# Kernel tuning notes

Measured on AMD Instinct MI355X. Metric: run time of the kernel, lower is better.

The kernel has to match this reference:

```python
import jax, jax.numpy as jnp
import numpy as np

H, W = 32, 32
C = 512
HEADS = 8
HEAD_DIM = C // HEADS
B = 8
GROUPS = 32
EPS = 1e-6
N = H * W


def _rel_indices():
    # (N, N) lookup indices into the (2H-1)*(2W-1) relative-position table
    y = np.arange(H)
    x = np.arange(W)
    y1, x1, y2, x2 = np.meshgrid(y, x, y, x, indexing='ij')
    idx = (y1 - y2 + H - 1) * (2 * W - 1) + (x1 - x2 + W - 1)
    return jnp.asarray(idx.reshape(N, N), dtype=jnp.int32)

REL_IDX = _rel_indices()


def setup_inputs() -> dict:
    key = jax.random.key(0)
    ks = jax.random.split(key, 8)
    s = 0.02
    return {
        'x': jax.random.normal(ks[0], (B, C, H, W), jnp.float32),
        '_1': jnp.zeros((1,), jnp.int32),
        '_2': jnp.zeros((1,), jnp.int32),
        'gamma': jnp.ones((C,), jnp.float32),
        'beta': jnp.zeros((C,), jnp.float32),
        'wq': jax.random.normal(ks[1], (C, C), jnp.float32) * s,
        'bq': jnp.zeros((C,), jnp.float32),
        'wk': jax.random.normal(ks[2], (C, C), jnp.float32) * s,
        'bk': jnp.zeros((C,), jnp.float32),
        'wv': jax.random.normal(ks[3], (C, C), jnp.float32) * s,
        'bv': jnp.zeros((C,), jnp.float32),
        'wproj': jax.random.normal(ks[4], (C, C), jnp.float32) * s,
        'bproj': jnp.zeros((C,), jnp.float32),
        'pos_enc': jax.random.normal(ks[5], (HEADS, (2 * H - 1) * (2 * W - 1)), jnp.float32) * s,
    }


def _group_norm(x, gamma, beta):
    b, c, h, w = x.shape
    xg = x.reshape(b, GROUPS, c // GROUPS, h, w)
    mean = xg.mean(axis=(2, 3, 4), keepdims=True)
    var = xg.var(axis=(2, 3, 4), keepdims=True)
    xg = (xg - mean) * jax.lax.rsqrt(var + EPS)
    x = xg.reshape(b, c, h, w)
    return x * gamma[None, :, None, None] + beta[None, :, None, None]


def reference(x, _1, _2, gamma, beta, wq, bq, wk, bk, wv, bv, wproj, bproj, pos_enc):
    x0 = x
    xn = _group_norm(x, gamma, beta)
    xt = xn.reshape(B, C, N)  # (B, C, N)

    def proj(w, bias):
        # 1x1 conv == channel matmul: (B, C_out, N)
        y = jnp.einsum('oc,bcn->bon', w, xt) + bias[None, :, None]
        # split heads: channel index = head*HEAD_DIM + d -> (B, heads, N, d)
        return y.reshape(B, HEADS, HEAD_DIM, N).transpose(0, 1, 3, 2)

    q = proj(wq, bq)
    k = proj(wk, bk)
    v = proj(wv, bv)

    scale = 1.0 / jnp.sqrt(jnp.float32(HEAD_DIM))
    attn = jnp.einsum('bhqd,bhkd->bhqk', q, k) * scale  # (B, heads, N, N)
    rel_bias = pos_enc[:, REL_IDX]  # (heads, N, N)
    attn = attn + rel_bias[None]
    attn = jax.nn.softmax(attn, axis=-1)

    out = jnp.einsum('bhqk,bhkd->bhqd', attn, v)  # (B, heads, N, d)
    out = out.transpose(0, 1, 3, 2).reshape(B, C, H, W)
    out = jnp.einsum('oc,bchw->bohw', wproj, out) + bproj[None, :, None, None]
    return out + x0
```

## Files before the change

### kernel.cpp

```cpp
#include <hip/hip_runtime.h>
#include <hip/hip_bf16.h>
#include <math.h>

typedef __bf16 bf16_t;
typedef __bf16 bf16x8 __attribute__((ext_vector_type(8)));
typedef __bf16 bf16x4 __attribute__((ext_vector_type(4)));
typedef float  f32x4  __attribute__((ext_vector_type(4)));

#define MFMA16(a, b, c) __builtin_amdgcn_mfma_f32_16x16x32_bf16((a), (b), (c), 0, 0, 0)
#define GLDS16(g, s) __builtin_amdgcn_global_load_lds( \
    (const __attribute__((address_space(1))) void*)(g), \
    (__attribute__((address_space(3))) void*)(s), 16, 0, 0)

#define LOG2E 1.4426950408889634f

__global__ __launch_bounds__(256) void cast_weights(
    const float* __restrict__ wq, const float* __restrict__ wk,
    const float* __restrict__ wv, const float* __restrict__ wp,
    bf16_t* __restrict__ Wqkv, bf16_t* __restrict__ Wp)
{
    const int i = (blockIdx.x * 256 + threadIdx.x) * 4;
#pragma unroll
    for (int j = 0; j < 4; ++j) {
        Wqkv[i + j]          = (bf16_t)wq[i + j];
        Wqkv[262144 + i + j] = (bf16_t)wk[i + j];
        Wqkv[524288 + i + j] = (bf16_t)wv[i + j];
        Wp[i + j]            = (bf16_t)wp[i + j];
    }
}

__global__ __launch_bounds__(256) void bias_kernel(
    const float* __restrict__ pos, bf16_t* __restrict__ Bias2)
{
    const int h   = blockIdx.x >> 6;
    const int qt  = blockIdx.x & 63;
    const int qy  = qt >> 1;
    const int qxb = (qt & 1) * 16;
    const int t = threadIdx.x;
    __shared__ bf16_t ps[32][64];

    for (int i = t; i < 32 * 63; i += 256) {
        const int r = i / 63, dx = i - r * 63;
        ps[r][dx] = (bf16_t)(pos[h * 3969 + (qy + r) * 63 + dx] * LOG2E);
    }
    __syncthreads();

    bf16_t* outb = Bias2 + (((size_t)h * 64 + qt) * 64) * 256;
#pragma unroll
    for (int it = 0; it < 16; ++it) {
        const int idx = t + it * 256;
        const int kt = idx >> 6, l = idx & 63;
        const int qx  = qxb + (l & 15);
        const int nk0 = kt * 16 + (l >> 4) * 4;
        const int ky = nk0 >> 5;
        const int kx0 = nk0 & 31;
        const int r = 31 - ky;
        const int dx0 = qx - kx0 + 31;
        bf16x4 o;
#pragma unroll
        for (int j = 0; j < 4; ++j) o[j] = ps[r][dx0 - j];
        *(bf16x4*)(outb + (size_t)idx * 4) = o;
    }
}

__global__ __launch_bounds__(512) void gn_kernel(
    const float* __restrict__ x, const float* __restrict__ gamma,
    const float* __restrict__ beta, bf16_t* __restrict__ xnT)
{
    const int blk = blockIdx.x;
    const int b = blk >> 5, g = blk & 31;
    const int t = threadIdx.x;
    const int hi = t >> 8, tl = t & 255;
    __shared__ float red[16];
    const float* base = x + ((size_t)b * 512 + g * 16) * 1024;

    f32x4 v[8];
    float s = 0.f, s2 = 0.f;
#pragma unroll
    for (int it = 0; it < 8; ++it) {
        v[it] = *(const f32x4*)(base + (size_t)hi * 8192 + it * 1024 + tl * 4);
#pragma unroll
        for (int j = 0; j < 4; ++j) { s += v[it][j]; s2 += v[it][j] * v[it][j]; }
    }
#pragma unroll
    for (int m = 1; m < 64; m <<= 1) { s += __shfl_xor(s, m); s2 += __shfl_xor(s2, m); }
    const int w = t >> 6;
    if ((t & 63) == 0) { red[w] = s; red[8 + w] = s2; }
    __syncthreads();
    s = 0.f; s2 = 0.f;
#pragma unroll
    for (int i = 0; i < 8; ++i) { s += red[i]; s2 += red[8 + i]; }
    const float mean = s * (1.f / 16384.f);
    const float var  = fmaxf(s2 * (1.f / 16384.f) - mean * mean, 0.f);
    const float rstd = rsqrtf(var + 1e-6f);

    float ga[8], be[8];
#pragma unroll
    for (int it = 0; it < 8; ++it) {
        const int gc = g * 16 + hi * 8 + it;
        ga[it] = gamma[gc] * rstd;
        be[it] = beta[gc] - mean * ga[it];
    }
#pragma unroll
    for (int j = 0; j < 4; ++j) {
        bf16x8 o;
#pragma unroll
        for (int it = 0; it < 8; ++it)
            o[it] = (bf16_t)(v[it][j] * ga[it] + be[it]);
        *(bf16x8*)(xnT + ((size_t)b * 1024 + tl * 4 + j) * 512 + g * 16 + hi * 8) = o;
    }
}

__global__ __launch_bounds__(256) void gemm_bt(
    const bf16_t* __restrict__ A, const bf16_t* __restrict__ Bt, int mode,
    int mtiles,
    const float* __restrict__ bias0, const float* __restrict__ bias1,
    const float* __restrict__ bias2,
    const float* __restrict__ x0, float* __restrict__ outF,
    bf16_t* __restrict__ Qb, bf16_t* __restrict__ Kb, bf16_t* __restrict__ Vb)
{
    const int K  = 512;
    const int g  = blockIdx.x;
    const int xcd = g & 7;
    const int i_  = g >> 3;
    const int m_idx = i_ % mtiles;
    const int n_idx = xcd * 8 + i_ / mtiles;
    const int m0 = m_idx * 128;
    const int n0 = n_idx * 128;
    const int t = threadIdx.x;
    const int l = t & 63, w = t >> 6;
    const int wr = w >> 1, wc = w & 1;
    const int lrow = l & 15, lgrp = l >> 4;

    __shared__ __align__(16) char smem_raw[49152];
    bf16_t* Ct = (bf16_t*)smem_raw;

    f32x4 acc[4][4];
#pragma unroll
    for (int i = 0; i < 4; ++i)
#pragma unroll
        for (int j = 0; j < 4; ++j) acc[i][j] = (f32x4){0.f, 0.f, 0.f, 0.f};

    const bf16_t* gA0 = A  + (size_t)(m0 + w * 16 + (l >> 2)) * K + (l & 3) * 8;
    const bf16_t* gA1 = gA0 + (size_t)64 * K;
    const bf16_t* gB0 = Bt + (size_t)(n0 + w * 16 + (l >> 2)) * K + (l & 3) * 8;
    const bf16_t* gB1 = gB0 + (size_t)64 * K;

#define STAGE(s, k0) do {                                                   \
    bf16_t* As_ = (bf16_t*)(smem_raw + (s) * 16384);                        \
    bf16_t* Bs_ = (bf16_t*)(smem_raw + (s) * 16384 + 8192);                 \
    GLDS16(gA0 + (k0), As_ + w * 512);                                      \
    GLDS16(gA1 + (k0), As_ + 2048 + w * 512);                               \
    GLDS16(gB0 + (k0), Bs_ + w * 512);                                      \
    GLDS16(gB1 + (k0), Bs_ + 2048 + w * 512); } while (0)

    STAGE(0, 0);
    STAGE(1, 32);

#pragma unroll
    for (int tk = 0; tk < 16; ++tk) {
        if (tk < 15) asm volatile("s_waitcnt vmcnt(4)" ::: "memory");
        else         asm volatile("s_waitcnt vmcnt(0)" ::: "memory");
        __builtin_amdgcn_s_barrier();
        __builtin_amdgcn_sched_barrier(0);
        if (tk + 2 < 16) STAGE((tk + 2) % 3, (tk + 2) * 32);
        const bf16_t* Asb = (const bf16_t*)(smem_raw + (tk % 3) * 16384);
        const bf16_t* Bsb = Asb + 4096;
        bf16x8 af[4], bfr[4];
#pragma unroll
        for (int ms = 0; ms < 4; ++ms)
            af[ms] = *(const bf16x8*)&Asb[(wr * 64 + ms * 16 + lrow) * 32 + lgrp * 8];
#pragma unroll
        for (int ns = 0; ns < 4; ++ns)
            bfr[ns] = *(const bf16x8*)&Bsb[(wc * 64 + ns * 16 + lrow) * 32 + lgrp * 8];
        __builtin_amdgcn_s_setprio(1);
#pragma unroll
        for (int ms = 0; ms < 4; ++ms)
#pragma unroll
            for (int ns = 0; ns < 4; ++ns)
                acc[ms][ns] = MFMA16(af[ms], bfr[ns], acc[ms][ns]);
        __builtin_amdgcn_s_setprio(0);
    }
#undef STAGE

    if (mode == 0) {
        const int which = m0 >> 9;
        const int mq = (m0 >> 7) & 3;
        const float* bias = (which == 0) ? bias0 : (which == 1) ? bias1 : bias2;
        const float scl = (which == 0) ? 0.125f * LOG2E : 1.0f;
        const int b   = n_idx >> 3;
        const int nn0 = (n_idx & 7) * 128;

        __syncthreads();
        if (which < 2) {
            bf16_t* Qk = (which == 0) ? Qb : Kb;
#pragma unroll
            for (int ms = 0; ms < 4; ++ms) {
                const int ml = wr * 64 + ms * 16 + lgrp * 4;
#pragma unroll
                for (int ns = 0; ns < 4; ++ns) {
                    const int nl = wc * 64 + ns * 16 + lrow;
                    bf16x4 pk;
#pragma unroll
                    for (int j = 0; j < 4; ++j)
                        pk[j] = (bf16_t)((acc[ms][ns][j] + bias[mq * 128 + ml + j]) * scl);
                    *(bf16x4*)&Ct[nl * 136 + ml] = pk;
                }
            }
            __syncthreads();
#pragma unroll
            for (int it = 0; it < 8; ++it) {
                const int idx = it * 256 + t;
                const int token = idx >> 4, oc = idx & 15;
                const bf16x8 vv8 = *(const bf16x8*)&Ct[token * 136 + oc * 8];
                const int head = mq * 2 + (oc >> 3);
                const int d = (oc & 7) * 8;
                *(bf16x8*)(Qk + (((size_t)b * 8 + head) * 1024 + nn0 + token) * 64 + d) = vv8;
            }
        } else {
#pragma unroll
            for (int ms = 0; ms < 4; ++ms) {
                const int ml = wr * 64 + ms * 16 + lgrp * 4;
#pragma unroll
                for (int ns = 0; ns < 4; ++ns) {
                    const int nl = wc * 64 + ns * 16 + lrow;
#pragma unroll
                    for (int j = 0; j < 4; ++j)
                        Ct[(ml + j) * 136 + nl] =
                            (bf16_t)(acc[ms][ns][j] + bias[mq * 128 + ml + j]);
                }
            }
            __syncthreads();
#pragma unroll
            for (int it = 0; it < 8; ++it) {
                const int idx = it * 256 + t;
                const int o = idx >> 4, nc = idx & 15;
                const bf16x8 vv8 = *(const bf16x8*)&Ct[o * 136 + nc * 8];
                const int head = mq * 2 + (o >> 6);
                const int d = o & 63;
                *(bf16x8*)(Vb + (((size_t)b * 8 + head) * 64 + d) * 1024 + nn0 + nc * 8) = vv8;
            }
        }
    } else {
#pragma unroll
        for (int ms = 0; ms < 4; ++ms) {
#pragma unroll
            for (int ns = 0; ns < 4; ++ns) {
                const int c  = m0 + wr * 64 + ms * 16 + lgrp * 4;
                const int np = n0 + wc * 64 + ns * 16 + lrow;
                const int b = np >> 10, n = np & 1023;
#pragma unroll
                for (int j = 0; j < 4; ++j) {
                    const size_t idx = ((size_t)b * 512 + c + j) * 1024 + n;
                    outF[idx] = acc[ms][ns][j] + bias0[c + j] + x0[idx];
                }
            }
        }
    }
}

__global__ __launch_bounds__(512) void attn_kernel(
    const bf16_t* __restrict__ Qb, const bf16_t* __restrict__ Kb,
    const bf16_t* __restrict__ Vb, const bf16_t* __restrict__ Bias2,
    bf16_t* __restrict__ Xo)
{
    const int bh = blockIdx.x;
    const int h  = bh & 7;
    const int q0 = blockIdx.y * 128;
    const int t = threadIdx.x;
    const int w = t >> 6, l = t & 63;
    const int lrow = l & 15, lgrp = l >> 4;

    __shared__ __align__(16) bf16_t Ks[128][72];
    __shared__ __align__(16) bf16_t Vs[64][136];
    __shared__ __align__(16) bf16_t Ps[8][16][72];

    const int qrow = q0 + w * 16 + lrow;
    const bf16_t* qbase = Qb + ((size_t)bh * 1024 + qrow) * 64;
    const bf16x8 qf0 = *(const bf16x8*)(qbase + lgrp * 8);
    const bf16x8 qf1 = *(const bf16x8*)(qbase + 32 + lgrp * 8);

    const bf16_t* bb = Bias2 + (((size_t)h * 64 + (q0 >> 4) + w) * 64) * 256;

    bf16x8 ones;
#pragma unroll
    for (int i = 0; i < 8; ++i) ones[i] = (bf16_t)1.0f;

    f32x4 oacc[4], tsacc = (f32x4){0.f, 0.f, 0.f, 0.f};
#pragma unroll
    for (int j = 0; j < 4; ++j) oacc[j] = (f32x4){0.f, 0.f, 0.f, 0.f};

    const int sr2 = t >> 3;
    const int sc2 = (t & 7) * 8;
    const bf16_t* Kg = Kb + ((size_t)bh * 1024 + sr2) * 64 + sc2;
    const bf16_t* Vg = Vb + ((size_t)bh * 64 + sr2) * 1024 + sc2;

    bf16x8 kv0 = *(const bf16x8*)(Kg);
    bf16x8 kv1 = *(const bf16x8*)(Kg + (size_t)64 * 64);
    bf16x8 vv0 = *(const bf16x8*)(Vg);
    bf16x8 vv1 = *(const bf16x8*)(Vg + 64);
    bf16x4 bA[8], bB[8];
#pragma unroll
    for (int k = 0; k < 8; ++k)
        bA[k] = *(const bf16x4*)(bb + (size_t)(k * 64 + l) * 4);

    auto dtile = [&](int it, bf16x4 (&bcur)[8], bf16x4 (&bnxt)[8]) {
        const int nk0 = it * 128;
        __syncthreads();
        *(bf16x8*)&Ks[sr2][sc2]      = kv0;
        *(bf16x8*)&Ks[64 + sr2][sc2] = kv1;
        *(bf16x8*)&Vs[sr2][sc2]      = vv0;
        *(bf16x8*)&Vs[sr2][64 + sc2] = vv1;
        __syncthreads();
        if (it < 7) {
            const int nkn = nk0 + 128;
#pragma unroll
            for (int k = 0; k < 8; ++k)
                bnxt[k] = *(const bf16x4*)(bb + (size_t)((((nkn >> 4)) + k) * 64 + l) * 4);
            kv0 = *(const bf16x8*)(Kg + (size_t)nkn * 64);
            kv1 = *(const bf16x8*)(Kg + (size_t)(nkn + 64) * 64);
            vv0 = *(const bf16x8*)(Vg + nkn);
            vv1 = *(const bf16x8*)(Vg + nkn + 64);
        }

#pragma unroll
        for (int st = 0; st < 2; ++st) {
            f32x4 s[4];
#pragma unroll
            for (int ns = 0; ns < 4; ++ns) {
                const bf16x4 bc = bcur[st * 4 + ns];
                f32x4 z = (f32x4){(float)bc[0], (float)bc[1],
                                  (float)bc[2], (float)bc[3]};
                const bf16x8 kf0 = *(const bf16x8*)&Ks[st * 64 + ns * 16 + lrow][lgrp * 8];
                const bf16x8 kf1 = *(const bf16x8*)&Ks[st * 64 + ns * 16 + lrow][32 + lgrp * 8];
                z = MFMA16(kf0, qf0, z);
                z = MFMA16(kf1, qf1, z);
                s[ns] = z;
            }
#pragma unroll
            for (int ns = 0; ns < 4; ++ns) {
                bf16x4 pk;
                pk[0] = (bf16_t)exp2f(s[ns][0]);
                pk[1] = (bf16_t)exp2f(s[ns][1]);
                pk[2] = (bf16_t)exp2f(s[ns][2]);
                pk[3] = (bf16_t)exp2f(s[ns][3]);
                *(bf16x4*)&Ps[w][lrow][ns * 16 + lgrp * 4] = pk;
            }
            const bf16x8 pf0 = *(const bf16x8*)&Ps[w][lrow][lgrp * 8];
            const bf16x8 pf1 = *(const bf16x8*)&Ps[w][lrow][32 + lgrp * 8];
            tsacc = MFMA16(ones, pf0, tsacc);
            tsacc = MFMA16(ones, pf1, tsacc);
#pragma unroll
            for (int ds = 0; ds < 4; ++ds) {
                const bf16x8 vf0 = *(const bf16x8*)&Vs[ds * 16 + lrow][st * 64 + lgrp * 8];
                const bf16x8 vf1 = *(const bf16x8*)&Vs[ds * 16 + lrow][st * 64 + 32 + lgrp * 8];
                oacc[ds] = MFMA16(vf0, pf0, oacc[ds]);
                oacc[ds] = MFMA16(vf1, pf1, oacc[ds]);
            }
        }
    };

    for (int it2 = 0; it2 < 8; it2 += 2) {
        dtile(it2,     bA, bB);
        dtile(it2 + 1, bB, bA);
    }

    const float inv = 1.0f / tsacc[0];

    const int b = bh >> 3;
    const int q = q0 + w * 16 + lrow;
    bf16_t* xrow = Xo + ((size_t)b * 1024 + q) * 512 + h * 64;
#pragma unroll
    for (int ds = 0; ds < 4; ++ds) {
        bf16x4 o4;
#pragma unroll
        for (int j = 0; j < 4; ++j) o4[j] = (bf16_t)(oacc[ds][j] * inv);
        *(bf16x4*)(xrow + ds * 16 + lgrp * 4) = o4;
    }
}

extern "C" void kernel_launch(void* const* d_in, const int* in_sizes, int n_in,
                              void* d_out, int out_size, void* d_ws, size_t ws_size,
                              hipStream_t stream)
{
    const float* x     = (const float*)d_in[0];
    const float* gamma = (const float*)d_in[3];
    const float* beta  = (const float*)d_in[4];
    const float* wq    = (const float*)d_in[5];
    const float* bq    = (const float*)d_in[6];
    const float* wk    = (const float*)d_in[7];
    const float* bk    = (const float*)d_in[8];
    const float* wv    = (const float*)d_in[9];
    const float* bv    = (const float*)d_in[10];
    const float* wp    = (const float*)d_in[11];
    const float* bp    = (const float*)d_in[12];
    const float* pos   = (const float*)d_in[13];
    float* out = (float*)d_out;

    size_t off = 0;
    char* wsb = (char*)d_ws;
    auto alloc = [&](size_t bytes) { char* p = wsb + off; off += bytes; return p; };
    bf16_t* Wqkv  = (bf16_t*)alloc((size_t)1536 * 512 * 2);
    bf16_t* Wp    = (bf16_t*)alloc((size_t)512 * 512 * 2);
    bf16_t* xnT   = (bf16_t*)alloc((size_t)8192 * 512 * 2);
    bf16_t* Qb    = (bf16_t*)alloc((size_t)8192 * 512 * 2);
    bf16_t* Kb    = (bf16_t*)alloc((size_t)8192 * 512 * 2);
    bf16_t* Vb    = (bf16_t*)alloc((size_t)8192 * 512 * 2);
    bf16_t* Xo    = (bf16_t*)alloc((size_t)8192 * 512 * 2);
    bf16_t* Bias2 = (bf16_t*)alloc((size_t)8 * 64 * 64 * 64 * 4 * 2);

    hipLaunchKernelGGL(cast_weights, dim3(256), dim3(256), 0, stream,
                       wq, wk, wv, wp, Wqkv, Wp);
    hipLaunchKernelGGL(bias_kernel, dim3(512), dim3(256), 0, stream, pos, Bias2);
    hipLaunchKernelGGL(gn_kernel, dim3(256), dim3(512), 0, stream,
                       x, gamma, beta, xnT);
    hipLaunchKernelGGL(gemm_bt, dim3(768), dim3(256), 0, stream,
                       Wqkv, xnT, 0, 12, bq, bk, bv,
                       nullptr, nullptr, Qb, Kb, Vb);
    hipLaunchKernelGGL(attn_kernel, dim3(64, 8), dim3(512), 0, stream,
                       Qb, Kb, Vb, Bias2, Xo);
    hipLaunchKernelGGL(gemm_bt, dim3(256), dim3(256), 0, stream,
                       Wp, Xo, 1, 4, bp, nullptr, nullptr,
                       x, out, nullptr, nullptr, nullptr);
}
```

Before: 93.67 us.

## Switch attention to 32x32 MFMA with register-resident P via permlane32 swap

The attention kernel now uses 32x32x16 MFMA tiles, so each wave handles 32 query rows and each block 256 queries. The probability tile no longer round-trips through LDS; it is packed and rearranged in registers with v_permlane32_swap. The bias table is laid out again to match the 32x32 accumulator layout, and the bias kernel is rewritten to produce it. This halves K/V reloads per query and drops the LDS P traffic, at the cost of more registers per thread and only 256 attention blocks.

```diff
diff --git a/kernel.cpp b/kernel.cpp
--- a/kernel.cpp
+++ b/kernel.cpp
@@ -5,9 +5,13 @@
 typedef __bf16 bf16_t;
 typedef __bf16 bf16x8 __attribute__((ext_vector_type(8)));
 typedef __bf16 bf16x4 __attribute__((ext_vector_type(4)));
+typedef __bf16 bf16x2 __attribute__((ext_vector_type(2)));
 typedef float  f32x4  __attribute__((ext_vector_type(4)));
+typedef float  f32x16 __attribute__((ext_vector_type(16)));
+typedef unsigned u32x4 __attribute__((ext_vector_type(4)));
 
 #define MFMA16(a, b, c) __builtin_amdgcn_mfma_f32_16x16x32_bf16((a), (b), (c), 0, 0, 0)
+#define MFMA32(a, b, c) __builtin_amdgcn_mfma_f32_32x32x16_bf16((a), (b), (c), 0, 0, 0)
 #define GLDS16(g, s) __builtin_amdgcn_global_load_lds( \
     (const __attribute__((address_space(1))) void*)(g), \
     (__attribute__((address_space(3))) void*)(s), 16, 0, 0)
@@ -30,36 +34,35 @@
 }
 
 __global__ __launch_bounds__(256) void bias_kernel(
-    const float* __restrict__ pos, bf16_t* __restrict__ Bias2)
-{
-    const int h   = blockIdx.x >> 6;
-    const int qt  = blockIdx.x & 63;
-    const int qy  = qt >> 1;
-    const int qxb = (qt & 1) * 16;
+    const float* __restrict__ pos, bf16_t* __restrict__ Bias3)
+{
+    const int h  = blockIdx.x >> 5;
+    const int qt = blockIdx.x & 31;
     const int t = threadIdx.x;
+    const int l = t & 63, ko = t >> 6;
     __shared__ bf16_t ps[32][64];
 
     for (int i = t; i < 32 * 63; i += 256) {
         const int r = i / 63, dx = i - r * 63;
-        ps[r][dx] = (bf16_t)(pos[h * 3969 + (qy + r) * 63 + dx] * LOG2E);
+        ps[r][dx] = (bf16_t)(pos[h * 3969 + (qt + r) * 63 + dx] * LOG2E);
     }
     __syncthreads();
 
-    bf16_t* outb = Bias2 + (((size_t)h * 64 + qt) * 64) * 256;
-#pragma unroll
-    for (int it = 0; it < 16; ++it) {
-        const int idx = t + it * 256;
-        const int kt = idx >> 6, l = idx & 63;
-        const int qx  = qxb + (l & 15);
-        const int nk0 = kt * 16 + (l >> 4) * 4;
-        const int ky = nk0 >> 5;
-        const int kx0 = nk0 & 31;
-        const int r = 31 - ky;
-        const int dx0 = qx - kx0 + 31;
-        bf16x4 o;
-#pragma unroll
-        for (int j = 0; j < 4; ++j) o[j] = ps[r][dx0 - j];
-        *(bf16x4*)(outb + (size_t)idx * 4) = o;
+    const int qx = l & 31, hi = l >> 5;
+#pragma unroll
+    for (int kt0 = 0; kt0 < 32; kt0 += 4) {
+        const int kt = kt0 + ko;
+        const int row = 31 - kt;
+        bf16x8 o0, o1;
+#pragma unroll
+        for (int reg = 0; reg < 16; ++reg) {
+            const int kx = (reg & 3) + 8 * (reg >> 2) + 4 * hi;
+            const bf16_t v = ps[row][qx - kx + 31];
+            if (reg < 8) o0[reg] = v; else o1[reg - 8] = v;
+        }
+        bf16_t* outp = Bias3 + ((size_t)(((h * 32 + qt) * 32 + kt) * 64 + l)) * 16;
+        *(bf16x8*)outp       = o0;
+        *(bf16x8*)(outp + 8) = o1;
     }
 }
 
@@ -259,36 +262,38 @@
     }
 }
 
-__global__ __launch_bounds__(512) void attn_kernel(
+__global__ __launch_bounds__(512, 2) void attn_kernel(
     const bf16_t* __restrict__ Qb, const bf16_t* __restrict__ Kb,
-    const bf16_t* __restrict__ Vb, const bf16_t* __restrict__ Bias2,
+    const bf16_t* __restrict__ Vb, const bf16_t* __restrict__ Bias3,
     bf16_t* __restrict__ Xo)
 {
     const int bh = blockIdx.x;
     const int h  = bh & 7;
-    const int q0 = blockIdx.y * 128;
+    const int q0 = blockIdx.y * 256;
     const int t = threadIdx.x;
     const int w = t >> 6, l = t & 63;
-    const int lrow = l & 15, lgrp = l >> 4;
+    const int lq = l & 31, hi = l >> 5;
 
     __shared__ __align__(16) bf16_t Ks[128][72];
     __shared__ __align__(16) bf16_t Vs[64][136];
-    __shared__ __align__(16) bf16_t Ps[8][16][72];
-
-    const int qrow = q0 + w * 16 + lrow;
+
+    const int qrow = q0 + w * 32 + lq;
     const bf16_t* qbase = Qb + ((size_t)bh * 1024 + qrow) * 64;
-    const bf16x8 qf0 = *(const bf16x8*)(qbase + lgrp * 8);
-    const bf16x8 qf1 = *(const bf16x8*)(qbase + 32 + lgrp * 8);
-
-    const bf16_t* bb = Bias2 + (((size_t)h * 64 + (q0 >> 4) + w) * 64) * 256;
+    bf16x8 qf[4];
+#pragma unroll
+    for (int dc = 0; dc < 4; ++dc)
+        qf[dc] = *(const bf16x8*)(qbase + dc * 16 + hi * 8);
+
+    const bf16_t* bbase = Bias3 +
+        ((size_t)((h * 32 + (q0 >> 5) + w) * 32)) * 1024 + (size_t)l * 16;
 
     bf16x8 ones;
 #pragma unroll
     for (int i = 0; i < 8; ++i) ones[i] = (bf16_t)1.0f;
 
-    f32x4 oacc[4], tsacc = (f32x4){0.f, 0.f, 0.f, 0.f};
-#pragma unroll
-    for (int j = 0; j < 4; ++j) oacc[j] = (f32x4){0.f, 0.f, 0.f, 0.f};
+    f32x16 oacc[2], tsacc;
+#pragma unroll
+    for (int j = 0; j < 16; ++j) { oacc[0][j] = 0.f; oacc[1][j] = 0.f; tsacc[j] = 0.f; }
 
     const int sr2 = t >> 3;
     const int sc2 = (t & 7) * 8;
@@ -299,12 +304,14 @@
     bf16x8 kv1 = *(const bf16x8*)(Kg + (size_t)64 * 64);
     bf16x8 vv0 = *(const bf16x8*)(Vg);
     bf16x8 vv1 = *(const bf16x8*)(Vg + 64);
-    bf16x4 bA[8], bB[8];
-#pragma unroll
-    for (int k = 0; k < 8; ++k)
-        bA[k] = *(const bf16x4*)(bb + (size_t)(k * 64 + l) * 4);
-
-    auto dtile = [&](int it, bf16x4 (&bcur)[8], bf16x4 (&bnxt)[8]) {
+    bf16x8 bA[8], bB[8];
+#pragma unroll
+    for (int k = 0; k < 4; ++k) {
+        bA[2 * k]     = *(const bf16x8*)(bbase + (size_t)k * 1024);
+        bA[2 * k + 1] = *(const bf16x8*)(bbase + (size_t)k * 1024 + 8);
+    }
+
+    auto dtile = [&](int it, bf16x8 (&bcur)[8], bf16x8 (&bnxt)[8]) {
         const int nk0 = it * 128;
         __syncthreads();
         *(bf16x8*)&Ks[sr2][sc2]      = kv0;
@@ -315,8 +322,10 @@
         if (it < 7) {
             const int nkn = nk0 + 128;
 #pragma unroll
-            for (int k = 0; k < 8; ++k)
-                bnxt[k] = *(const bf16x4*)(bb + (size_t)((((nkn >> 4)) + k) * 64 + l) * 4);
+            for (int k = 0; k < 4; ++k) {
+                bnxt[2 * k]     = *(const bf16x8*)(bbase + (size_t)((it + 1) * 4 + k) * 1024);
+                bnxt[2 * k + 1] = *(const bf16x8*)(bbase + (size_t)((it + 1) * 4 + k) * 1024 + 8);
+            }
             kv0 = *(const bf16x8*)(Kg + (size_t)nkn * 64);
             kv1 = *(const bf16x8*)(Kg + (size_t)(nkn + 64) * 64);
             vv0 = *(const bf16x8*)(Vg + nkn);
@@ -324,38 +333,48 @@
         }
 
 #pragma unroll
-        for (int st = 0; st < 2; ++st) {
-            f32x4 s[4];
-#pragma unroll
-            for (int ns = 0; ns < 4; ++ns) {
-                const bf16x4 bc = bcur[st * 4 + ns];
-                f32x4 z = (f32x4){(float)bc[0], (float)bc[1],
-                                  (float)bc[2], (float)bc[3]};
-                const bf16x8 kf0 = *(const bf16x8*)&Ks[st * 64 + ns * 16 + lrow][lgrp * 8];
-                const bf16x8 kf1 = *(const bf16x8*)&Ks[st * 64 + ns * 16 + lrow][32 + lgrp * 8];
-                z = MFMA16(kf0, qf0, z);
-                z = MFMA16(kf1, qf1, z);
-                s[ns] = z;
-            }
-#pragma unroll
-            for (int ns = 0; ns < 4; ++ns) {
-                bf16x4 pk;
-                pk[0] = (bf16_t)exp2f(s[ns][0]);
-                pk[1] = (bf16_t)exp2f(s[ns][1]);
-                pk[2] = (bf16_t)exp2f(s[ns][2]);
-                pk[3] = (bf16_t)exp2f(s[ns][3]);
-                *(bf16x4*)&Ps[w][lrow][ns * 16 + lgrp * 4] = pk;
-            }
-            const bf16x8 pf0 = *(const bf16x8*)&Ps[w][lrow][lgrp * 8];
-            const bf16x8 pf1 = *(const bf16x8*)&Ps[w][lrow][32 + lgrp * 8];
-            tsacc = MFMA16(ones, pf0, tsacc);
-            tsacc = MFMA16(ones, pf1, tsacc);
-#pragma unroll
-            for (int ds = 0; ds < 4; ++ds) {
-                const bf16x8 vf0 = *(const bf16x8*)&Vs[ds * 16 + lrow][st * 64 + lgrp * 8];
-                const bf16x8 vf1 = *(const bf16x8*)&Vs[ds * 16 + lrow][st * 64 + 32 + lgrp * 8];
-                oacc[ds] = MFMA16(vf0, pf0, oacc[ds]);
-                oacc[ds] = MFMA16(vf1, pf1, oacc[ds]);
+        for (int kt = 0; kt < 4; ++kt) {
+            const int ktloc = kt * 32;
+            f32x16 sa;
+#pragma unroll
+            for (int r = 0; r < 8; ++r) {
+                sa[r]     = (float)bcur[2 * kt][r];
+                sa[8 + r] = (float)bcur[2 * kt + 1][r];
+            }
+#pragma unroll
+            for (int dc = 0; dc < 4; ++dc) {
+                const bf16x8 kf = *(const bf16x8*)&Ks[ktloc + lq][dc * 16 + hi * 8];
+                sa = MFMA32(kf, qf[dc], sa);
+            }
+            unsigned W00, W01, W10, W11, W20, W21, W30, W31;
+            {
+                float p[16];
+#pragma unroll
+                for (int r = 0; r < 16; ++r) p[r] = exp2f(sa[r]);
+                bf16x2 tw;
+#define PACKW(dst, a, b_) { tw[0] = (bf16_t)p[a]; tw[1] = (bf16_t)p[b_]; \
+                            dst = __builtin_bit_cast(unsigned, tw); }
+                PACKW(W00, 0, 1)   PACKW(W01, 2, 3)
+                PACKW(W10, 4, 5)   PACKW(W11, 6, 7)
+                PACKW(W20, 8, 9)   PACKW(W21, 10, 11)
+                PACKW(W30, 12, 13) PACKW(W31, 14, 15)
+#undef PACKW
+            }
+            asm volatile("v_permlane32_swap_b32 %0, %1" : "+v"(W00), "+v"(W10));
+            asm volatile("v_permlane32_swap_b32 %0, %1" : "+v"(W01), "+v"(W11));
+            asm volatile("v_permlane32_swap_b32 %0, %1" : "+v"(W20), "+v"(W30));
+            asm volatile("v_permlane32_swap_b32 %0, %1" : "+v"(W21), "+v"(W31));
+            const bf16x8 pf0 = __builtin_bit_cast(bf16x8, (u32x4){W00, W01, W10, W11});
+            const bf16x8 pf1 = __builtin_bit_cast(bf16x8, (u32x4){W20, W21, W30, W31});
+
+            tsacc = MFMA32(ones, pf0, tsacc);
+            tsacc = MFMA32(ones, pf1, tsacc);
+#pragma unroll
+            for (int dh = 0; dh < 2; ++dh) {
+                const bf16x8 vf0 = *(const bf16x8*)&Vs[dh * 32 + lq][ktloc + hi * 8];
+                const bf16x8 vf1 = *(const bf16x8*)&Vs[dh * 32 + lq][ktloc + 16 + hi * 8];
+                oacc[dh] = MFMA32(vf0, pf0, oacc[dh]);
+                oacc[dh] = MFMA32(vf1, pf1, oacc[dh]);
             }
         }
     };
@@ -368,15 +387,18 @@
     const float inv = 1.0f / tsacc[0];
 
     const int b = bh >> 3;
-    const int q = q0 + w * 16 + lrow;
+    const int q = q0 + w * 32 + lq;
     bf16_t* xrow = Xo + ((size_t)b * 1024 + q) * 512 + h * 64;
 #pragma unroll
-    for (int ds = 0; ds < 4; ++ds) {
-        bf16x4 o4;
-#pragma unroll
-        for (int j = 0; j < 4; ++j) o4[j] = (bf16_t)(oacc[ds][j] * inv);
-        *(bf16x4*)(xrow + ds * 16 + lgrp * 4) = o4;
-    }
+    for (int dh = 0; dh < 2; ++dh)
+#pragma unroll
+        for (int rr = 0; rr < 4; ++rr) {
+            bf16x4 o4;
+#pragma unroll
+            for (int j = 0; j < 4; ++j)
+                o4[j] = (bf16_t)(oacc[dh][4 * rr + j] * inv);
+            *(bf16x4*)(xrow + dh * 32 + 8 * rr + 4 * hi) = o4;
+        }
 }
 
 extern "C" void kernel_launch(void* const* d_in, const int* in_sizes, int n_in,
@@ -407,18 +429,18 @@
     bf16_t* Kb    = (bf16_t*)alloc((size_t)8192 * 512 * 2);
     bf16_t* Vb    = (bf16_t*)alloc((size_t)8192 * 512 * 2);
     bf16_t* Xo    = (bf16_t*)alloc((size_t)8192 * 512 * 2);
-    bf16_t* Bias2 = (bf16_t*)alloc((size_t)8 * 64 * 64 * 64 * 4 * 2);
+    bf16_t* Bias3 = (bf16_t*)alloc((size_t)8 * 32 * 32 * 64 * 16 * 2);
 
     hipLaunchKernelGGL(cast_weights, dim3(256), dim3(256), 0, stream,
                        wq, wk, wv, wp, Wqkv, Wp);
-    hipLaunchKernelGGL(bias_kernel, dim3(512), dim3(256), 0, stream, pos, Bias2);
+    hipLaunchKernelGGL(bias_kernel, dim3(256), dim3(256), 0, stream, pos, Bias3);
     hipLaunchKernelGGL(gn_kernel, dim3(256), dim3(512), 0, stream,
                        x, gamma, beta, xnT);
     hipLaunchKernelGGL(gemm_bt, dim3(768), dim3(256), 0, stream,
                        Wqkv, xnT, 0, 12, bq, bk, bv,
                        nullptr, nullptr, Qb, Kb, Vb);
-    hipLaunchKernelGGL(attn_kernel, dim3(64, 8), dim3(512), 0, stream,
-                       Qb, Kb, Vb, Bias2, Xo);
+    hipLaunchKernelGGL(attn_kernel, dim3(64, 4), dim3(512), 0, stream,
+                       Qb, Kb, Vb, Bias3, Xo);
     hipLaunchKernelGGL(gemm_bt, dim3(256), dim3(256), 0, stream,
                        Wp, Xo, 1, 4, bp, nullptr, nullptr,
                        x, out, nullptr, nullptr, nullptr);
```

Measured after the change: 93.19 us. About the same (-0.5%).
